# Kernel optimization log

Hardware: AMD Instinct MI355X
Metric: run time of the kernel (lower is better)

Reference implementation:

```python
import jax, jax.numpy as jnp
import numpy as np

S = 128          # voxel grid resolution per axis
NPB = 50000      # active voxels per batch element
B = 2            # batch size
C_IN = 64
C_OUT = 64
K = 3            # kernel size

# kernel offsets in [-1,0,1]^3, shape [27, 3]
_OFFS = np.stack(np.meshgrid(np.arange(-1, 2), np.arange(-1, 2), np.arange(-1, 2), indexing='ij'), axis=-1).reshape(-1, 3)


def setup_inputs() -> dict:
    rng = np.random.default_rng(0)
    coords_list = []
    for b in range(B):
        lin = rng.choice(S * S * S, size=NPB, replace=False)  # unique voxels
        x = lin // (S * S)
        y = (lin // S) % S
        z = lin % S
        coords_list.append(np.stack([np.full(NPB, b), x, y, z], axis=1))
    coords = jnp.asarray(np.concatenate(coords_list, axis=0), dtype=jnp.int32)  # [N,4]

    key = jax.random.key(0)
    k1, k2, k3 = jax.random.split(key, 3)
    feats = jax.random.normal(k1, (B * NPB, C_IN), dtype=jnp.float32)
    fan1 = C_IN * K ** 3
    fan2 = C_OUT * K ** 3
    W1 = jax.random.normal(k2, (K ** 3, C_IN, C_OUT), dtype=jnp.float32) / np.sqrt(fan1)
    W2 = jax.random.normal(k3, (K ** 3, C_OUT, C_OUT), dtype=jnp.float32) / np.sqrt(fan2)
    return {"feats": feats, "coords": coords, "W1": W1, "W2": W2}


def _encode(coords):
    # linear key: ((b*S + x)*S + y)*S + z ; fits in int32 for S=128, B small
    b, x, y, z = coords[:, 0], coords[:, 1], coords[:, 2], coords[:, 3]
    return ((b * S + x) * S + y) * S + z


def _sparse_conv(feats, coords, W):
    """Stride-1 sparse (submanifold-style) 3D conv: output coords == input coords.
    feats [N,Cin], coords [N,4], W [27,Cin,Cout] -> [N,Cout]."""
    N = feats.shape[0]
    keys = _encode(coords)
    order = jnp.argsort(keys)
    skeys = keys[order]
    offs = jnp.asarray(_OFFS, dtype=jnp.int32)  # [27,3]

    def gather_one(d):
        qxyz = coords[:, 1:4] + d[None, :]
        valid = jnp.all((qxyz >= 0) & (qxyz < S), axis=1)
        qkey = keys + (d[0] * S * S + d[1] * S + d[2])
        idx = jnp.clip(jnp.searchsorted(skeys, qkey), 0, N - 1)
        found = valid & (skeys[idx] == qkey)
        return jnp.where(found[:, None], feats[order[idx]], 0.0)  # [N,Cin]

    gathered = jax.vmap(gather_one)(offs)  # [27, N, Cin]
    return jnp.einsum('onc,ocd->nd', gathered, W)


def reference(feats, coords, W1, W2):
    h = _sparse_conv(feats, coords, W1)
    out = _sparse_conv(h, coords, W2)
    return out
```

## Files before the change

### kernel.cpp

```cpp
#include <hip/hip_runtime.h>
#include <stdint.h>

#define SGRID 128
#define CAP 4096

typedef _Float16 f16;
typedef f16 f16x8 __attribute__((ext_vector_type(8)));
typedef float f32x4 __attribute__((ext_vector_type(4)));
typedef unsigned long long u64;

static __device__ __forceinline__ f32x4 mfma16(uint4 a, uint4 b, f32x4 c) {
    union { uint4 u; f16x8 v; } ua, ub;
    ua.u = a; ub.u = b;
    return __builtin_amdgcn_mfma_f32_16x16x32_f16(ua.v, ub.v, c, 0, 0, 0);
}

static __device__ __forceinline__ void split8(const float* v, uint4& hu, uint4& lu) {
    union { f16 h[8]; uint4 u; } hv, lv;
    #pragma unroll
    for (int j = 0; j < 8; ++j) {
        f16 h = (f16)v[j];
        hv.h[j] = h;
        lv.h[j] = (f16)(v[j] - (float)h);
    }
    hu = hv.u; lu = lv.u;
}

static __device__ __forceinline__ void gload16(const void* g, void* l) {
    __builtin_amdgcn_global_load_lds(
        (const __attribute__((address_space(1))) unsigned int*)g,
        (__attribute__((address_space(3))) unsigned int*)l, 16, 0, 0);
}

static __device__ __forceinline__ void read_row_frags(
    const float* __restrict__ sW, int rl, int lq, uint4 ah[2], uint4 al[2])
{
    #pragma unroll
    for (int ks = 0; ks < 2; ++ks) {
        int c0 = ks * 8 + lq * 2;
        int s0 = (c0 - rl) & 15, s1 = (c0 + 1 - rl) & 15;
        float4 v0 = *(const float4*)&sW[(rl * 16 + s0) * 4];
        float4 v1 = *(const float4*)&sW[(rl * 16 + s1) * 4];
        float v[8] = {v0.x, v0.y, v0.z, v0.w, v1.x, v1.y, v1.z, v1.w};
        split8(v, ah[ks], al[ks]);
    }
}

static __device__ __forceinline__ void center_staged(
    const float* __restrict__ A, const uint4 b[2][4], float* __restrict__ O,
    int N, int gw0, int tid, float* sF)
{
    const int w = tid >> 6, lane = tid & 63;
    const int r = lane & 15, lq = lane >> 4;
    const int gw = gw0 + w;
    const int p0 = gw * 32;
    float* sW = sF + w * 2048;

    #pragma unroll
    for (int j = 0; j < 8; ++j) {
        int ch = j * 64 + lane;
        int rl = ch >> 4, slot = ch & 15;
        int csrc = (slot + rl) & 15;
        int grow = p0 + rl;
        if (grow > N - 1) grow = N - 1;
        gload16(A + (size_t)grow * 64 + csrc * 4, sW + j * 256);
    }
    asm volatile("s_waitcnt vmcnt(0)" ::: "memory");
    __builtin_amdgcn_sched_barrier(0);
    if (p0 >= N) return;

    uint4 ah[2][2], al[2][2];
    #pragma unroll
    for (int rt = 0; rt < 2; ++rt)
        read_row_frags(sW, rt * 16 + r, lq, ah[rt], al[rt]);

    f32x4 acc[2][4];
    #pragma unroll
    for (int i = 0; i < 2; ++i)
        #pragma unroll
        for (int j = 0; j < 4; ++j) acc[i][j] = (f32x4){0.f, 0.f, 0.f, 0.f};

    #pragma unroll
    for (int ks = 0; ks < 2; ++ks)
        #pragma unroll
        for (int rt = 0; rt < 2; ++rt)
            #pragma unroll
            for (int ct = 0; ct < 4; ++ct) {
                acc[rt][ct] = mfma16(ah[rt][ks], b[ks][ct], acc[rt][ct]);
                acc[rt][ct] = mfma16(al[rt][ks], b[ks][ct], acc[rt][ct]);
            }

    #pragma unroll
    for (int rt = 0; rt < 2; ++rt)
        #pragma unroll
        for (int j = 0; j < 4; ++j) {
            int row = p0 + rt * 16 + lq * 4 + j;
            if (row < N) {
                #pragma unroll
                for (int ct = 0; ct < 4; ++ct)
                    O[(size_t)row * 64 + ct * 16 + r] = acc[rt][ct][j];
            }
        }
}

static __device__ __forceinline__ void build_body(
    const int* __restrict__ coords, const int* __restrict__ table,
    const unsigned* __restrict__ bitmap,
    int* __restrict__ pin, int* __restrict__ pout, int* __restrict__ cnt,
    int N, int ck, int tid, u64 (*sbal)[4], int (*sbase4)[4])
{
    const int lane = tid & 63, wave = tid >> 6;
    const int n = ck * 256 + tid;
    const bool valid = n < N;

    int4 c = {0, 0, 0, 0};
    if (valid) c = ((const int4*)coords)[n];
    const int z  = c.w;
    const int zb = (z == 0) ? 0 : z - 1;
    const int wofs = zb >> 5, sh = zb & 31;

    unsigned omask = 0;
    #pragma unroll
    for (int cidx = 0; cidx < 9; ++cidx) {
        int dx = cidx / 3 - 1, dy = cidx % 3 - 1;
        int qx = c.y + dx, qy = c.z + dy;
        bool colok = valid && ((unsigned)qx < SGRID) && ((unsigned)qy < SGRID);
        int wi = colok ? ((((c.x * SGRID + qx) * SGRID + qy) << 2) + wofs) : 0;
        unsigned w0 = bitmap[wi];
        unsigned w1 = bitmap[wi + 1];
        u64 w = (u64)w0 | ((u64)w1 << 32);
        unsigned t = (unsigned)(w >> sh) & 7u;
        if (z == 0)         t = (t << 1) & 6u;
        if (z == SGRID - 1) t &= 3u;
        t = colok ? t : 0u;
        omask |= t << (cidx * 3);
    }
    omask &= ~(1u << 13);

    const int key = ((c.x * SGRID + c.y) * SGRID + c.z) * SGRID + z;
    int nb[26];
    #pragma unroll
    for (int s = 0; s < 26; ++s) {
        int o = s < 13 ? s : s + 1;
        bool occ = (omask >> o) & 1u;
        int qkey = key + (o / 9 - 1) * SGRID * SGRID + ((o / 3) % 3 - 1) * SGRID + (o % 3 - 1);
        int v = table[occ ? qkey : 0];
        nb[s] = occ ? v : -1;
    }

    #pragma unroll
    for (int s = 0; s < 26; ++s) {
        u64 bal = __ballot(nb[s] >= 0);
        if (lane == 0) sbal[s][wave] = bal;
    }
    __syncthreads();

    if (tid < 26) {
        int c0 = (int)__popcll(sbal[tid][0]);
        int c1 = (int)__popcll(sbal[tid][1]);
        int c2 = (int)__popcll(sbal[tid][2]);
        int c3 = (int)__popcll(sbal[tid][3]);
        int tot = c0 + c1 + c2 + c3;
        int base = tot ? atomicAdd(&cnt[tid * 16], tot) : 0;
        sbase4[tid][0] = base;
        sbase4[tid][1] = base + c0;
        sbase4[tid][2] = base + c0 + c1;
        sbase4[tid][3] = base + c0 + c1 + c2;
    }
    __syncthreads();

    const u64 ltmask = (1ull << lane) - 1ull;
    #pragma unroll
    for (int s = 0; s < 26; ++s) {
        if (nb[s] >= 0) {
            int pos = sbase4[s][wave] + (int)__popcll(sbal[s][wave] & ltmask);
            if (pos < CAP) {
                pin[s * CAP + pos]  = nb[s];
                pout[s * CAP + pos] = n;
            }
        }
    }
}

static __device__ __forceinline__ void wprep_item(
    const float* __restrict__ W1, const float* __restrict__ W2,
    f16* __restrict__ Wp1, f16* __restrict__ Wp2, int idx)
{
    const int half = 27 * 512;
    const float* W = (idx < half) ? W1 : W2;
    f16* Wp = (idx < half) ? Wp1 : Wp2;
    int id = (idx < half) ? idx : idx - half;
    int lane = id & 63;
    int ks = (id >> 6) & 1;
    int ct = (id >> 7) & 3;
    int o  = id >> 9;
    int co  = ct * 16 + (lane & 15);
    int ci0 = ks * 32 + (lane >> 4) * 8;
    union { f16 h[8]; uint4 u; } hv;
    #pragma unroll
    for (int j = 0; j < 8; ++j)
        hv.h[j] = (f16)W[((size_t)o * 64 + ci0 + j) * 64 + co];
    ((uint4*)Wp)[id] = hv.u;
}

__global__ void clear_meta(uint4* __restrict__ bitmap4, int nwords4,
                           int* __restrict__ cnt, float* __restrict__ zrow) {
    const int stride = gridDim.x * 256;
    for (int i = blockIdx.x * 256 + threadIdx.x; i < nwords4; i += stride)
        bitmap4[i] = (uint4){0, 0, 0, 0};
    if (blockIdx.x == 0 && threadIdx.x < 26) cnt[threadIdx.x * 16] = 0;
    if (blockIdx.x == 0 && threadIdx.x < 64) zrow[threadIdx.x] = 0.f;
}

__global__ void __launch_bounds__(256) scatter_prep(
    const int* __restrict__ coords, int* __restrict__ table,
    unsigned* __restrict__ bitmap, int N, int scatB,
    const float* __restrict__ W1, const float* __restrict__ W2,
    f16* __restrict__ Wp1, f16* __restrict__ Wp2)
{
    const int tid = threadIdx.x;
    if (blockIdx.x < scatB) {
        int i = blockIdx.x * 256 + tid;
        if (i < N) {
            int4 c = ((const int4*)coords)[i];
            int key = ((c.x * SGRID + c.y) * SGRID + c.z) * SGRID + c.w;
            table[key] = i;
            atomicOr(&bitmap[key >> 5], 1u << (key & 31));
        }
        return;
    }
    wprep_item(W1, W2, Wp1, Wp2, (blockIdx.x - scatB) * 256 + tid);
}

__global__ void __launch_bounds__(256) build_center(
    const int* __restrict__ coords, const int* __restrict__ table,
    const unsigned* __restrict__ bitmap,
    int* __restrict__ pin, int* __restrict__ pout, int* __restrict__ cnt,
    int N, int probeB,
    const float* __restrict__ F, const f16* __restrict__ Wp, float* __restrict__ H)
{
    __shared__ union {
        float sF[8192];
        struct { u64 sbal[26][4]; int sbase4[26][4]; } pb;
    } sm;

    if (blockIdx.x >= probeB) {
        const int lane = threadIdx.x & 63;
        const uint4* wb = (const uint4*)Wp + 13 * 512 + lane;
        uint4 b[2][4];
        #pragma unroll
        for (int ct = 0; ct < 4; ++ct)
            #pragma unroll
            for (int ks = 0; ks < 2; ++ks)
                b[ks][ct] = wb[(ct * 2 + ks) * 64];
        center_staged(F, b, H, N, (blockIdx.x - probeB) * 4, threadIdx.x, sm.sF);
        return;
    }
    build_body(coords, table, bitmap, pin, pout, cnt, N, blockIdx.x, threadIdx.x,
               sm.pb.sbal, sm.pb.sbase4);
}

__global__ void __launch_bounds__(256) conv_center(
    const float* __restrict__ A, const f16* __restrict__ Wp,
    float* __restrict__ O, int N)
{
    __shared__ float sF[8192];
    const int lane = threadIdx.x & 63;
    const uint4* wb = (const uint4*)Wp + 13 * 512 + lane;
    uint4 b[2][4];
    #pragma unroll
    for (int ct = 0; ct < 4; ++ct)
        #pragma unroll
        for (int ks = 0; ks < 2; ++ks)
            b[ks][ct] = wb[(ct * 2 + ks) * 64];
    center_staged(A, b, O, N, blockIdx.x * 4, threadIdx.x, sF);
}

__global__ void __launch_bounds__(256) conv_sparse(
    const float* __restrict__ A, const f16* __restrict__ Wp,
    const int* __restrict__ pin, const int* __restrict__ pout,
    const int* __restrict__ cnt, float* __restrict__ O,
    const float* __restrict__ zrow)
{
    __shared__ float sF[4096];
    int w = (blockIdx.x * 256 + threadIdx.x) >> 6;
    if (w >= 26 * 512) return;
    const int lane = threadIdx.x & 63;
    const int wv = threadIdx.x >> 6;
    int slot  = w >> 9;
    int rem   = w & 511;
    int chunk = rem >> 1;
    int ch    = rem & 1;
    int cn = cnt[slot * 16]; if (cn > CAP) cn = CAP;
    int i0 = chunk * 16;
    if (i0 >= cn) return;
    int o = slot < 13 ? slot : slot + 1;
    const int r = lane & 15, lq = lane >> 4;
    float* sW = sF + wv * 1024;

    #pragma unroll
    for (int i = 0; i < 4; ++i) {
        int rl = i * 4 + (lane >> 4);
        int slotc = lane & 15;
        int csrc = (slotc + rl) & 15;
        int p = i0 + rl;
        const float* src;
        if (p < cn) {
            int rid = pin[slot * CAP + p];
            src = A + (size_t)rid * 64 + csrc * 4;
        } else {
            src = zrow + csrc * 4;
        }
        gload16(src, sW + i * 256);
    }

    const uint4* wb = (const uint4*)Wp + (size_t)o * 512 + lane;
    uint4 b[2][2];
    #pragma unroll
    for (int ct = 0; ct < 2; ++ct)
        #pragma unroll
        for (int ks = 0; ks < 2; ++ks)
            b[ct][ks] = wb[((ch * 2 + ct) * 2 + ks) * 64];

    asm volatile("s_waitcnt vmcnt(0)" ::: "memory");
    __builtin_amdgcn_sched_barrier(0);

    uint4 ah[2], al[2];
    read_row_frags(sW, r, lq, ah, al);

    f32x4 acc[2];
    acc[0] = (f32x4){0.f, 0.f, 0.f, 0.f};
    acc[1] = (f32x4){0.f, 0.f, 0.f, 0.f};
    #pragma unroll
    for (int ks = 0; ks < 2; ++ks)
        #pragma unroll
        for (int ct = 0; ct < 2; ++ct) {
            acc[ct] = mfma16(ah[ks], b[ct][ks], acc[ct]);
            acc[ct] = mfma16(al[ks], b[ct][ks], acc[ct]);
        }

    #pragma unroll
    for (int j = 0; j < 4; ++j) {
        int pr = i0 + lq * 4 + j;
        if (pr < cn) {
            int oidx = pout[slot * CAP + pr];
            #pragma unroll
            for (int ct = 0; ct < 2; ++ct)
                atomicAdd(&O[(size_t)oidx * 64 + (ch * 2 + ct) * 16 + r], acc[ct][j]);
        }
    }
}

extern "C" void kernel_launch(void* const* d_in, const int* in_sizes, int n_in,
                              void* d_out, int out_size, void* d_ws, size_t ws_size,
                              hipStream_t stream) {
    const float* feats  = (const float*)d_in[0];
    const int*   coords = (const int*)d_in[1];
    const float* W1     = (const float*)d_in[2];
    const float* W2     = (const float*)d_in[3];
    float* out = (float*)d_out;

    const int N = in_sizes[0] / 64;
    const size_t nvox = 2ull * SGRID * SGRID * SGRID;

    char* p = (char*)d_ws;
    int*      table  = (int*)p;      p += nvox * 4;
    unsigned* bitmap = (unsigned*)p; p += (nvox / 32) * 4;
    p += 16;
    int*      cnt    = (int*)p;      p += 26 * 16 * 4;
    float*    zrow   = (float*)p;    p += 64 * 4;
    int*      pin    = (int*)p;      p += 26ull * CAP * 4;
    int*      pout   = (int*)p;      p += 26ull * CAP * 4;
    float*    H      = (float*)p;    p += (size_t)N * 64 * 4;
    f16*      Wp1    = (f16*)p;      p += 27ull * 4096 * 2;
    f16*      Wp2    = (f16*)p;      p += 27ull * 4096 * 2;

    const int bm4     = (int)(nvox / 32 / 4) + 1;
    const int scatB   = (N + 255) / 256;
    const int ngroups = (N + 31) / 32;
    const int centerB = (ngroups + 3) / 4;
    const int sparseB = 26 * 512 / 4;

    clear_meta<<<256, 256, 0, stream>>>((uint4*)bitmap, bm4, cnt, zrow);
    scatter_prep<<<scatB + 108, 256, 0, stream>>>(coords, table, bitmap, N, scatB,
                                                  W1, W2, Wp1, Wp2);
    build_center<<<scatB + centerB, 256, 0, stream>>>(coords, table, bitmap,
                                                      pin, pout, cnt, N, scatB,
                                                      feats, Wp1, H);
    conv_sparse<<<sparseB, 256, 0, stream>>>(feats, Wp1, pin, pout, cnt, H, zrow);
    conv_center<<<centerB, 256, 0, stream>>>(H, Wp2, out, N);
    conv_sparse<<<sparseB, 256, 0, stream>>>(H, Wp2, pin, pout, cnt, out, zrow);
}
```

Baseline: 95.05 us.

## Replace atomic scatter of sparse-offset products with partial buffer and per-row gather

Sparse-offset GEMM results are no longer atomically added into the output. They are written to a dense partial buffer indexed by (offset, pair position). A new center kernel then computes the center-offset product and gathers each row's partials, using a per-row offset mask and a position table built during map construction. Each sparse wave now covers all 64 output channels instead of 32. This removes float atomics and the dependence on pre-zeroed or pre-written output. The cost is extra partial-buffer traffic, extra map arrays, and a serial per-row gather loop with scattered reads.

```diff
diff --git a/kernel.cpp b/kernel.cpp
--- a/kernel.cpp
+++ b/kernel.cpp
@@ -8,6 +8,7 @@
 typedef f16 f16x8 __attribute__((ext_vector_type(8)));
 typedef float f32x4 __attribute__((ext_vector_type(4)));
 typedef unsigned long long u64;
+typedef unsigned short u16;
 
 static __device__ __forceinline__ f32x4 mfma16(uint4 a, uint4 b, f32x4 c) {
     union { uint4 u; f16x8 v; } ua, ub;
@@ -46,71 +47,61 @@
     }
 }
 
-static __device__ __forceinline__ void center_staged(
-    const float* __restrict__ A, const uint4 b[2][4], float* __restrict__ O,
-    int N, int gw0, int tid, float* sF)
-{
-    const int w = tid >> 6, lane = tid & 63;
-    const int r = lane & 15, lq = lane >> 4;
-    const int gw = gw0 + w;
-    const int p0 = gw * 32;
-    float* sW = sF + w * 2048;
-
-    #pragma unroll
-    for (int j = 0; j < 8; ++j) {
-        int ch = j * 64 + lane;
-        int rl = ch >> 4, slot = ch & 15;
-        int csrc = (slot + rl) & 15;
-        int grow = p0 + rl;
-        if (grow > N - 1) grow = N - 1;
-        gload16(A + (size_t)grow * 64 + csrc * 4, sW + j * 256);
-    }
-    asm volatile("s_waitcnt vmcnt(0)" ::: "memory");
-    __builtin_amdgcn_sched_barrier(0);
-    if (p0 >= N) return;
-
-    uint4 ah[2][2], al[2][2];
-    #pragma unroll
-    for (int rt = 0; rt < 2; ++rt)
-        read_row_frags(sW, rt * 16 + r, lq, ah[rt], al[rt]);
-
-    f32x4 acc[2][4];
-    #pragma unroll
-    for (int i = 0; i < 2; ++i)
-        #pragma unroll
-        for (int j = 0; j < 4; ++j) acc[i][j] = (f32x4){0.f, 0.f, 0.f, 0.f};
-
-    #pragma unroll
-    for (int ks = 0; ks < 2; ++ks)
-        #pragma unroll
-        for (int rt = 0; rt < 2; ++rt)
-            #pragma unroll
-            for (int ct = 0; ct < 4; ++ct) {
-                acc[rt][ct] = mfma16(ah[rt][ks], b[ks][ct], acc[rt][ct]);
-                acc[rt][ct] = mfma16(al[rt][ks], b[ks][ct], acc[rt][ct]);
-            }
-
-    #pragma unroll
-    for (int rt = 0; rt < 2; ++rt)
-        #pragma unroll
-        for (int j = 0; j < 4; ++j) {
-            int row = p0 + rt * 16 + lq * 4 + j;
-            if (row < N) {
-                #pragma unroll
-                for (int ct = 0; ct < 4; ++ct)
-                    O[(size_t)row * 64 + ct * 16 + r] = acc[rt][ct][j];
-            }
-        }
-}
-
-static __device__ __forceinline__ void build_body(
+__global__ void k_clear(uint4* __restrict__ bitmap4, int nwords4,
+                        int* __restrict__ cnt, float* __restrict__ zrow) {
+    const int stride = gridDim.x * 256;
+    for (int i = blockIdx.x * 256 + threadIdx.x; i < nwords4; i += stride)
+        bitmap4[i] = (uint4){0, 0, 0, 0};
+    if (blockIdx.x == 0 && threadIdx.x < 26) cnt[threadIdx.x * 16] = 0;
+    if (blockIdx.x == 0 && threadIdx.x < 64) zrow[threadIdx.x] = 0.f;
+}
+
+__global__ void __launch_bounds__(256) k_scatprep(
+    const int* __restrict__ coords, int* __restrict__ table,
+    unsigned* __restrict__ bitmap, int N, int scatB,
+    const float* __restrict__ W1, const float* __restrict__ W2,
+    f16* __restrict__ Wp1, f16* __restrict__ Wp2)
+{
+    const int tid = threadIdx.x;
+    if (blockIdx.x < scatB) {
+        int i = blockIdx.x * 256 + tid;
+        if (i < N) {
+            int4 c = ((const int4*)coords)[i];
+            int key = ((c.x * SGRID + c.y) * SGRID + c.z) * SGRID + c.w;
+            table[key] = i;
+            atomicOr(&bitmap[key >> 5], 1u << (key & 31));
+        }
+        return;
+    }
+    int idx = (blockIdx.x - scatB) * 256 + tid;
+    const int half = 27 * 512;
+    const float* W = (idx < half) ? W1 : W2;
+    f16* Wp = (idx < half) ? Wp1 : Wp2;
+    int id = (idx < half) ? idx : idx - half;
+    int lane = id & 63;
+    int ks = (id >> 6) & 1;
+    int ct = (id >> 7) & 3;
+    int o  = id >> 9;
+    int co  = ct * 16 + (lane & 15);
+    int ci0 = ks * 32 + (lane >> 4) * 8;
+    union { f16 h[8]; uint4 u; } hv;
+    #pragma unroll
+    for (int j = 0; j < 8; ++j)
+        hv.h[j] = (f16)W[((size_t)o * 64 + ci0 + j) * 64 + co];
+    ((uint4*)Wp)[id] = hv.u;
+}
+
+__global__ void __launch_bounds__(256) k_build(
     const int* __restrict__ coords, const int* __restrict__ table,
     const unsigned* __restrict__ bitmap,
-    int* __restrict__ pin, int* __restrict__ pout, int* __restrict__ cnt,
-    int N, int ck, int tid, u64 (*sbal)[4], int (*sbase4)[4])
-{
-    const int lane = tid & 63, wave = tid >> 6;
-    const int n = ck * 256 + tid;
+    int* __restrict__ pin, u16* __restrict__ ppos, unsigned* __restrict__ omaskA,
+    int* __restrict__ cnt, int N)
+{
+    __shared__ u64 sbal[26][4];
+    __shared__ int sbase4[26][4];
+
+    const int tid = threadIdx.x, lane = tid & 63, wave = tid >> 6;
+    const int n = blockIdx.x * 256 + tid;
     const bool valid = n < N;
 
     int4 c = {0, 0, 0, 0};
@@ -170,127 +161,33 @@
     __syncthreads();
 
     const u64 ltmask = (1ull << lane) - 1ull;
+    unsigned fm = 0;
     #pragma unroll
     for (int s = 0; s < 26; ++s) {
         if (nb[s] >= 0) {
             int pos = sbase4[s][wave] + (int)__popcll(sbal[s][wave] & ltmask);
             if (pos < CAP) {
-                pin[s * CAP + pos]  = nb[s];
-                pout[s * CAP + pos] = n;
+                pin[s * CAP + pos] = nb[s];
+                ppos[(size_t)s * N + n] = (u16)pos;
+                fm |= 1u << s;
             }
         }
     }
-}
-
-static __device__ __forceinline__ void wprep_item(
-    const float* __restrict__ W1, const float* __restrict__ W2,
-    f16* __restrict__ Wp1, f16* __restrict__ Wp2, int idx)
-{
-    const int half = 27 * 512;
-    const float* W = (idx < half) ? W1 : W2;
-    f16* Wp = (idx < half) ? Wp1 : Wp2;
-    int id = (idx < half) ? idx : idx - half;
-    int lane = id & 63;
-    int ks = (id >> 6) & 1;
-    int ct = (id >> 7) & 3;
-    int o  = id >> 9;
-    int co  = ct * 16 + (lane & 15);
-    int ci0 = ks * 32 + (lane >> 4) * 8;
-    union { f16 h[8]; uint4 u; } hv;
-    #pragma unroll
-    for (int j = 0; j < 8; ++j)
-        hv.h[j] = (f16)W[((size_t)o * 64 + ci0 + j) * 64 + co];
-    ((uint4*)Wp)[id] = hv.u;
-}
-
-__global__ void clear_meta(uint4* __restrict__ bitmap4, int nwords4,
-                           int* __restrict__ cnt, float* __restrict__ zrow) {
-    const int stride = gridDim.x * 256;
-    for (int i = blockIdx.x * 256 + threadIdx.x; i < nwords4; i += stride)
-        bitmap4[i] = (uint4){0, 0, 0, 0};
-    if (blockIdx.x == 0 && threadIdx.x < 26) cnt[threadIdx.x * 16] = 0;
-    if (blockIdx.x == 0 && threadIdx.x < 64) zrow[threadIdx.x] = 0.f;
-}
-
-__global__ void __launch_bounds__(256) scatter_prep(
-    const int* __restrict__ coords, int* __restrict__ table,
-    unsigned* __restrict__ bitmap, int N, int scatB,
-    const float* __restrict__ W1, const float* __restrict__ W2,
-    f16* __restrict__ Wp1, f16* __restrict__ Wp2)
-{
-    const int tid = threadIdx.x;
-    if (blockIdx.x < scatB) {
-        int i = blockIdx.x * 256 + tid;
-        if (i < N) {
-            int4 c = ((const int4*)coords)[i];
-            int key = ((c.x * SGRID + c.y) * SGRID + c.z) * SGRID + c.w;
-            table[key] = i;
-            atomicOr(&bitmap[key >> 5], 1u << (key & 31));
-        }
-        return;
-    }
-    wprep_item(W1, W2, Wp1, Wp2, (blockIdx.x - scatB) * 256 + tid);
-}
-
-__global__ void __launch_bounds__(256) build_center(
-    const int* __restrict__ coords, const int* __restrict__ table,
-    const unsigned* __restrict__ bitmap,
-    int* __restrict__ pin, int* __restrict__ pout, int* __restrict__ cnt,
-    int N, int probeB,
-    const float* __restrict__ F, const f16* __restrict__ Wp, float* __restrict__ H)
-{
-    __shared__ union {
-        float sF[8192];
-        struct { u64 sbal[26][4]; int sbase4[26][4]; } pb;
-    } sm;
-
-    if (blockIdx.x >= probeB) {
-        const int lane = threadIdx.x & 63;
-        const uint4* wb = (const uint4*)Wp + 13 * 512 + lane;
-        uint4 b[2][4];
-        #pragma unroll
-        for (int ct = 0; ct < 4; ++ct)
-            #pragma unroll
-            for (int ks = 0; ks < 2; ++ks)
-                b[ks][ct] = wb[(ct * 2 + ks) * 64];
-        center_staged(F, b, H, N, (blockIdx.x - probeB) * 4, threadIdx.x, sm.sF);
-        return;
-    }
-    build_body(coords, table, bitmap, pin, pout, cnt, N, blockIdx.x, threadIdx.x,
-               sm.pb.sbal, sm.pb.sbase4);
-}
-
-__global__ void __launch_bounds__(256) conv_center(
+    if (valid) omaskA[n] = fm;
+}
+
+__global__ void __launch_bounds__(256) k_spart(
     const float* __restrict__ A, const f16* __restrict__ Wp,
-    float* __restrict__ O, int N)
-{
-    __shared__ float sF[8192];
-    const int lane = threadIdx.x & 63;
-    const uint4* wb = (const uint4*)Wp + 13 * 512 + lane;
-    uint4 b[2][4];
-    #pragma unroll
-    for (int ct = 0; ct < 4; ++ct)
-        #pragma unroll
-        for (int ks = 0; ks < 2; ++ks)
-            b[ks][ct] = wb[(ct * 2 + ks) * 64];
-    center_staged(A, b, O, N, blockIdx.x * 4, threadIdx.x, sF);
-}
-
-__global__ void __launch_bounds__(256) conv_sparse(
-    const float* __restrict__ A, const f16* __restrict__ Wp,
-    const int* __restrict__ pin, const int* __restrict__ pout,
-    const int* __restrict__ cnt, float* __restrict__ O,
-    const float* __restrict__ zrow)
+    const int* __restrict__ pin, const int* __restrict__ cnt,
+    float* __restrict__ P, const float* __restrict__ zrow)
 {
     __shared__ float sF[4096];
     int w = (blockIdx.x * 256 + threadIdx.x) >> 6;
-    if (w >= 26 * 512) return;
+    if (w >= 26 * 256) return;
     const int lane = threadIdx.x & 63;
     const int wv = threadIdx.x >> 6;
-    int slot  = w >> 9;
-    int rem   = w & 511;
-    int chunk = rem >> 1;
-    int ch    = rem & 1;
+    int slot  = w >> 8;
+    int chunk = w & 255;
     int cn = cnt[slot * 16]; if (cn > CAP) cn = CAP;
     int i0 = chunk * 16;
     if (i0 >= cn) return;
@@ -315,12 +212,12 @@
     }
 
     const uint4* wb = (const uint4*)Wp + (size_t)o * 512 + lane;
-    uint4 b[2][2];
-    #pragma unroll
-    for (int ct = 0; ct < 2; ++ct)
+    uint4 b[2][4];
+    #pragma unroll
+    for (int ct = 0; ct < 4; ++ct)
         #pragma unroll
         for (int ks = 0; ks < 2; ++ks)
-            b[ct][ks] = wb[((ch * 2 + ct) * 2 + ks) * 64];
+            b[ks][ct] = wb[(ct * 2 + ks) * 64];
 
     asm volatile("s_waitcnt vmcnt(0)" ::: "memory");
     __builtin_amdgcn_sched_barrier(0);
@@ -328,27 +225,112 @@
     uint4 ah[2], al[2];
     read_row_frags(sW, r, lq, ah, al);
 
-    f32x4 acc[2];
-    acc[0] = (f32x4){0.f, 0.f, 0.f, 0.f};
-    acc[1] = (f32x4){0.f, 0.f, 0.f, 0.f};
+    f32x4 acc[4];
+    #pragma unroll
+    for (int ct = 0; ct < 4; ++ct) acc[ct] = (f32x4){0.f, 0.f, 0.f, 0.f};
     #pragma unroll
     for (int ks = 0; ks < 2; ++ks)
         #pragma unroll
-        for (int ct = 0; ct < 2; ++ct) {
-            acc[ct] = mfma16(ah[ks], b[ct][ks], acc[ct]);
-            acc[ct] = mfma16(al[ks], b[ct][ks], acc[ct]);
+        for (int ct = 0; ct < 4; ++ct) {
+            acc[ct] = mfma16(ah[ks], b[ks][ct], acc[ct]);
+            acc[ct] = mfma16(al[ks], b[ks][ct], acc[ct]);
         }
 
     #pragma unroll
     for (int j = 0; j < 4; ++j) {
         int pr = i0 + lq * 4 + j;
-        if (pr < cn) {
-            int oidx = pout[slot * CAP + pr];
+        float* dst = P + ((size_t)(slot * CAP + pr) << 6);
+        #pragma unroll
+        for (int ct = 0; ct < 4; ++ct)
+            dst[ct * 16 + r] = acc[ct][j];
+    }
+}
+
+__global__ void __launch_bounds__(256) k_cgather(
+    const float* __restrict__ A, const f16* __restrict__ Wp,
+    const unsigned* __restrict__ omaskA, const u16* __restrict__ ppos,
+    const float* __restrict__ P, float* __restrict__ O, int N)
+{
+    __shared__ float sF[8192];
+    const int tid = threadIdx.x;
+    const int wv = tid >> 6, lane = tid & 63;
+    const int r = lane & 15, lq = lane >> 4;
+    const int gw = blockIdx.x * 4 + wv;
+    const int p0 = gw * 32;
+    float* sW = sF + wv * 2048;
+
+    #pragma unroll
+    for (int j = 0; j < 8; ++j) {
+        int ch = j * 64 + lane;
+        int rl = ch >> 4, slot = ch & 15;
+        int csrc = (slot + rl) & 15;
+        int grow = p0 + rl;
+        if (grow > N - 1) grow = N - 1;
+        gload16(A + (size_t)grow * 64 + csrc * 4, sW + j * 256);
+    }
+
+    const uint4* wb = (const uint4*)Wp + 13 * 512 + lane;
+    uint4 b[2][4];
+    #pragma unroll
+    for (int ct = 0; ct < 4; ++ct)
+        #pragma unroll
+        for (int ks = 0; ks < 2; ++ks)
+            b[ks][ct] = wb[(ct * 2 + ks) * 64];
+
+    asm volatile("s_waitcnt vmcnt(0)" ::: "memory");
+    __builtin_amdgcn_sched_barrier(0);
+    if (p0 >= N) return;
+
+    uint4 ah[2][2], al[2][2];
+    #pragma unroll
+    for (int rt = 0; rt < 2; ++rt)
+        read_row_frags(sW, rt * 16 + r, lq, ah[rt], al[rt]);
+
+    f32x4 acc[2][4];
+    #pragma unroll
+    for (int i = 0; i < 2; ++i)
+        #pragma unroll
+        for (int j = 0; j < 4; ++j) acc[i][j] = (f32x4){0.f, 0.f, 0.f, 0.f};
+
+    #pragma unroll
+    for (int ks = 0; ks < 2; ++ks)
+        #pragma unroll
+        for (int rt = 0; rt < 2; ++rt)
             #pragma unroll
-            for (int ct = 0; ct < 2; ++ct)
-                atomicAdd(&O[(size_t)oidx * 64 + (ch * 2 + ct) * 16 + r], acc[ct][j]);
-        }
-    }
+            for (int ct = 0; ct < 4; ++ct) {
+                acc[rt][ct] = mfma16(ah[rt][ks], b[ks][ct], acc[rt][ct]);
+                acc[rt][ct] = mfma16(al[rt][ks], b[ks][ct], acc[rt][ct]);
+            }
+
+    #pragma unroll
+    for (int rt = 0; rt < 2; ++rt)
+        #pragma unroll
+        for (int j = 0; j < 4; ++j) {
+            int row = p0 + rt * 16 + lq * 4 + j;
+            if (row < N) {
+                unsigned om = omaskA[row];
+                while (om) {
+                    int s = __ffs(om) - 1; om &= om - 1;
+                    int pos = ppos[(size_t)s * N + row];
+                    const float* pr_ = P + ((size_t)(s * CAP + pos) << 6);
+                    #pragma unroll
+                    for (int ct = 0; ct < 4; ++ct)
+                        acc[rt][ct][j] += pr_[ct * 16 + r];
+                }
+            }
+        }
+
+    #pragma unroll
+    for (int rt = 0; rt < 2; ++rt)
+        #pragma unroll
+        for (int j = 0; j < 4; ++j) {
+            int row = p0 + rt * 16 + lq * 4 + j;
+            if (row < N) {
+                #pragma unroll
+                for (int ct = 0; ct < 4; ++ct)
+                    O[(size_t)row * 64 + ct * 16 + r] = acc[rt][ct][j];
+            }
+        }
 }
 
 extern "C" void kernel_launch(void* const* d_in, const int* in_sizes, int n_in,
@@ -370,7 +352,9 @@
     int*      cnt    = (int*)p;      p += 26 * 16 * 4;
     float*    zrow   = (float*)p;    p += 64 * 4;
     int*      pin    = (int*)p;      p += 26ull * CAP * 4;
-    int*      pout   = (int*)p;      p += 26ull * CAP * 4;
+    u16*      ppos   = (u16*)p;      p += ((26ull * N * 2 + 15) & ~15ull);
+    unsigned* omaskA = (unsigned*)p; p += (size_t)N * 4;
+    float*    partial= (float*)p;    p += 26ull * CAP * 64 * 4;
     float*    H      = (float*)p;    p += (size_t)N * 64 * 4;
     f16*      Wp1    = (f16*)p;      p += 27ull * 4096 * 2;
     f16*      Wp2    = (f16*)p;      p += 27ull * 4096 * 2;
@@ -379,15 +363,14 @@
     const int scatB   = (N + 255) / 256;
     const int ngroups = (N + 31) / 32;
     const int centerB = (ngroups + 3) / 4;
-    const int sparseB = 26 * 512 / 4;
-
-    clear_meta<<<256, 256, 0, stream>>>((uint4*)bitmap, bm4, cnt, zrow);
-    scatter_prep<<<scatB + 108, 256, 0, stream>>>(coords, table, bitmap, N, scatB,
-                                                  W1, W2, Wp1, Wp2);
-    build_center<<<scatB + centerB, 256, 0, stream>>>(coords, table, bitmap,
-                                                      pin, pout, cnt, N, scatB,
-                                                      feats, Wp1, H);
-    conv_sparse<<<sparseB, 256, 0, stream>>>(feats, Wp1, pin, pout, cnt, H, zrow);
-    conv_center<<<centerB, 256, 0, stream>>>(H, Wp2, out, N);
-    conv_sparse<<<sparseB, 256, 0, stream>>>(H, Wp2, pin, pout, cnt, out, zrow);
-}
+    const int spartB  = 26 * 256 / 4;
+
+    k_clear<<<256, 256, 0, stream>>>((uint4*)bitmap, bm4, cnt, zrow);
+    k_scatprep<<<scatB + 108, 256, 0, stream>>>(coords, table, bitmap, N, scatB,
+                                                W1, W2, Wp1, Wp2);
+    k_build<<<scatB, 256, 0, stream>>>(coords, table, bitmap, pin, ppos, omaskA, cnt, N);
+    k_spart<<<spartB, 256, 0, stream>>>(feats, Wp1, pin, cnt, partial, zrow);
+    k_cgather<<<centerB, 256, 0, stream>>>(feats, Wp1, omaskA, ppos, partial, H, N);
+    k_spart<<<spartB, 256, 0, stream>>>(H, Wp2, pin, cnt, partial, zrow);
+    k_cgather<<<centerB, 256, 0, stream>>>(H, Wp2, omaskA, ppos, partial, out, N);
+}
```

New measurement: 99.68 us. +4.9%, slower.
